# Kernel tuning notes

Hardware: AMD Instinct MI355X
Metric: run time of the kernel (lower is better)

Reference implementation:

```python
import jax, jax.numpy as jnp
import numpy as np

FRAMES = 8
NUM_HEADS = 12


def _build_indices_mask(N_origin):
    """Static (numpy) construction of gathered token indices and the
    multiplicative token mask (1.0 on allowed pairs, 0.8 elsewhere),
    matching token_mask + (1-token_mask)*0.8 in the torch code."""
    N = FRAMES * N_origin
    cls_idx = np.arange(0, N, N_origin)
    per_frame = [np.arange(i * N_origin + 1 + i, (i + 1) * N_origin, FRAMES)
                 for i in range(FRAMES)]
    idx = np.concatenate([cls_idx] + per_frame)
    M = idx.shape[0]
    mask = np.full((N, M), 0.8, dtype=np.float32)
    cls_len = cls_idx.shape[0]
    mask[:, :cls_len] = 1.0
    st = cls_len
    for i in range(FRAMES):
        ln = per_frame[i].shape[0]
        mask[i * N_origin:(i + 1) * N_origin, st:st + ln] = 1.0
        st += ln
    return jnp.asarray(idx), jnp.asarray(mask)


def setup_inputs() -> dict:
    key = jax.random.key(0)
    k1, k2, k3, k4 = jax.random.split(key, 4)
    C = 768
    x = jax.random.normal(k1, (64, 197, C), dtype=jnp.float32)
    qkv_w = jax.random.normal(k2, (3 * C, C), dtype=jnp.float32) * 0.02
    proj_w = jax.random.normal(k3, (C, C), dtype=jnp.float32) * 0.02
    proj_b = jax.random.normal(k4, (C,), dtype=jnp.float32) * 0.02
    return {"x": x, "qkv_w": qkv_w, "proj_w": proj_w, "proj_b": proj_b}


def reference(x, qkv_w, proj_w, proj_b):
    B0, N_origin, C = x.shape
    H = NUM_HEADS
    hd = C // H
    B = B0 // FRAMES
    N = FRAMES * N_origin
    scale = hd ** -0.5

    xg = x.reshape(B, N, C)                              # group 8 frames per video
    qkv = (xg @ qkv_w.T).reshape(B, N, 3, H, hd).transpose(2, 0, 3, 1, 4)
    q, k, v = qkv[0], qkv[1], qkv[2]                     # each [B, H, N, hd]

    idx, mask = _build_indices_mask(N_origin)            # idx [M], mask [N, M]
    k = k[:, :, idx, :]                                  # [B, H, M, hd]
    v = v[:, :, idx, :]

    attn = jnp.einsum('bhnd,bhmd->bhnm', q, k) * scale   # [B, H, N, M]
    attn = jax.nn.softmax(attn * mask, axis=-1)          # multiplicative mask, then softmax

    out = jnp.einsum('bhnm,bhmd->bhnd', attn, v)         # [B, H, N, hd]
    out = out.transpose(0, 2, 1, 3).reshape(B, N, C)
    out = out @ proj_w.T + proj_b
    return out.reshape(B0, N_origin, C)
```

## Files before the change

### kernel.cpp

```cpp
#include <hip/hip_runtime.h>
#include <stdint.h>

#define NORI   197
#define FRAMES 8
#define NTOK   1576
#define BATCH  8
#define NHEAD  12
#define CDIM   768
#define MG     204
#define TOKENS 12608

typedef _Float16 half8 __attribute__((ext_vector_type(8)));
typedef float floatx4 __attribute__((ext_vector_type(4)));

typedef const __attribute__((address_space(1))) void GPTR;
typedef __attribute__((address_space(3))) void LPTR;

__device__ __forceinline__ int gather_idx(int m) {
    if (m < 8) return m * NORI;
    int u = m - 8;
    int f, t;
    if (u < 100) { f = u / 25; t = u - f * 25; }
    else         { f = 4 + (u - 100) / 24; t = (u - 100) - (f - 4) * 24; }
    return f * NORI + 1 + f + 8 * t;
}
__device__ __forceinline__ int col_frame(int m) {
    int u = m - 8;
    return (u < 100) ? (u / 25) : (4 + (u - 100) / 24);
}

__global__ __launch_bounds__(256) void cast_all(
    const float* __restrict__ x, const float* __restrict__ qkvw,
    const float* __restrict__ projw, _Float16* __restrict__ out)
{
    const int n1 = TOKENS * CDIM / 8, n2 = 3 * CDIM * CDIM / 8, n3 = CDIM * CDIM / 8;
    int i = blockIdx.x * 256 + threadIdx.x;
    if (i >= n1 + n2 + n3) return;
    const float* src; int off;
    if (i < n1)           { src = x;     off = i; }
    else if (i < n1 + n2) { src = qkvw;  off = i - n1; }
    else                  { src = projw; off = i - n1 - n2; }
    float4 a = ((const float4*)src)[2 * off];
    float4 b = ((const float4*)src)[2 * off + 1];
    half8 o = { (_Float16)a.x, (_Float16)a.y, (_Float16)a.z, (_Float16)a.w,
                (_Float16)b.x, (_Float16)b.y, (_Float16)b.z, (_Float16)b.w };
    ((half8*)out)[i] = o;
}

template <int OUT_F32>
__device__ __forceinline__ void gemm_body64(
    const _Float16* __restrict__ A, const _Float16* __restrict__ W,
    const float* __restrict__ bias, void* __restrict__ Y,
    int M, int Woff, int ldY, int gather, int r0, int c0,
    _Float16* As0, _Float16* Bs0, _Float16* As1, _Float16* Bs1)
{
    const int tid = threadIdx.x;
    const int w = tid >> 6, l = tid & 63;
    const int wm = (w >> 1) * 32, wn = (w & 1) * 64;
    const int cg = (l & 3) ^ ((l >> 3) & 3);

    const _Float16* saA;
    {
        int rt = w * 16 + (l >> 2);
        int ra = min(r0 + rt, M - 1);
        if (gather) { int b = ra / MG; int m = ra - b * MG; ra = b * NTOK + gather_idx(m); }
        saA = A + (size_t)ra * CDIM + cg * 8;
    }
    const int soffA = (w * 16) * 32;

    const _Float16* sb[2];
    int soffB[2];
#pragma unroll
    for (int i = 0; i < 2; i++) {
        int rt = w * 32 + i * 16 + (l >> 2);
        sb[i] = W + (size_t)(Woff + c0 + rt) * CDIM + cg * 8;
        soffB[i] = (w * 32 + i * 16) * 32;
    }

    __builtin_amdgcn_global_load_lds((GPTR*)saA, (LPTR*)(As0 + soffA), 16, 0, 0);
#pragma unroll
    for (int i = 0; i < 2; i++)
        __builtin_amdgcn_global_load_lds((GPTR*)sb[i], (LPTR*)(Bs0 + soffB[i]), 16, 0, 0);

    floatx4 acc[2][4] = {};
    const int fc = ((l >> 4) ^ ((l >> 1) & 3)) * 8;
    const int mrow = l & 15;
    const int lm = l & 15, lq = l >> 4;

#pragma unroll
    for (int it = 0; it < 24; it++) {
        const _Float16* Ac = (it & 1) ? As1 : As0;
        const _Float16* Bc = (it & 1) ? Bs1 : Bs0;
        _Float16* An = (it & 1) ? As0 : As1;
        _Float16* Bn = (it & 1) ? Bs0 : Bs1;

        if (it < 23) {
            int kb = (it + 1) * 32;
            __builtin_amdgcn_global_load_lds((GPTR*)(saA + kb), (LPTR*)(An + soffA), 16, 0, 0);
#pragma unroll
            for (int i = 0; i < 2; i++)
                __builtin_amdgcn_global_load_lds((GPTR*)(sb[i] + kb), (LPTR*)(Bn + soffB[i]), 16, 0, 0);
            __builtin_amdgcn_s_waitcnt(0x0073);
        } else {
            __builtin_amdgcn_s_waitcnt(0x0070);
        }
        __builtin_amdgcn_s_barrier();
        __builtin_amdgcn_sched_barrier(0);

        half8 af[2], bf[4];
#pragma unroll
        for (int t = 0; t < 2; t++)
            af[t] = *(const half8*)&Ac[(wm + t * 16 + mrow) * 32 + fc];
#pragma unroll
        for (int t = 0; t < 4; t++)
            bf[t] = *(const half8*)&Bc[(wn + t * 16 + mrow) * 32 + fc];
#pragma unroll
        for (int mt = 0; mt < 2; mt++)
#pragma unroll
            for (int nt = 0; nt < 4; nt++)
                acc[mt][nt] = __builtin_amdgcn_mfma_f32_16x16x32_f16(af[mt], bf[nt], acc[mt][nt], 0, 0, 0);

        __builtin_amdgcn_sched_barrier(0);
        __builtin_amdgcn_s_barrier();
    }

#pragma unroll
    for (int nt = 0; nt < 4; nt++) {
        int col = c0 + wn + nt * 16 + lm;
        float bv = bias ? bias[col] : 0.f;
#pragma unroll
        for (int mt = 0; mt < 2; mt++) {
#pragma unroll
            for (int r = 0; r < 4; r++) {
                int row = r0 + wm + mt * 16 + lq * 4 + r;
                if (row < M) {
                    if (OUT_F32) ((float*)Y)[(size_t)row * ldY + col] = acc[mt][nt][r] + bv;
                    else ((_Float16*)Y)[(size_t)row * ldY + col] = (_Float16)acc[mt][nt][r];
                }
            }
        }
    }
}

__device__ __forceinline__ int xcd_chunk(int bid, int nwg) {
    int xcd = bid & 7, j = bid >> 3;
    int q = nwg >> 3, r = nwg & 7;
    int base = (xcd < r) ? xcd * (q + 1) : r * (q + 1) + (xcd - r) * q;
    return base + j;
}

__global__ __launch_bounds__(256, 5) void gemm_qkv(
    const _Float16* __restrict__ xh, const _Float16* __restrict__ qkvwh,
    _Float16* __restrict__ Qh, _Float16* __restrict__ KVh)
{
    __shared__ __align__(16) _Float16 As0[64 * 32];
    __shared__ __align__(16) _Float16 Bs0[128 * 32];
    __shared__ __align__(16) _Float16 As1[64 * 32];
    __shared__ __align__(16) _Float16 Bs1[128 * 32];
    int bx = blockIdx.x;
    if (bx < 1182) {
        int wg = xcd_chunk(bx, 1182);
        int rb = wg / 6, cb = wg - rb * 6;
        gemm_body64<0>(xh, qkvwh, nullptr, Qh, TOKENS, 0, CDIM, 0,
                       rb * 64, cb * 128, As0, Bs0, As1, Bs1);
    } else {
        int b2 = bx - 1182;
        int wg = xcd_chunk(b2, 312);
        int rb = wg / 12, cb = wg - rb * 12;
        gemm_body64<0>(xh, qkvwh, nullptr, KVh, BATCH * MG, CDIM, 1536, 1,
                       rb * 64, cb * 128, As0, Bs0, As1, Bs1);
    }
}

__global__ __launch_bounds__(256, 5) void gemm_proj(
    const _Float16* __restrict__ AOh, const _Float16* __restrict__ projwh,
    const float* __restrict__ bias, float* __restrict__ out)
{
    __shared__ __align__(16) _Float16 As0[64 * 32];
    __shared__ __align__(16) _Float16 Bs0[128 * 32];
    __shared__ __align__(16) _Float16 As1[64 * 32];
    __shared__ __align__(16) _Float16 Bs1[128 * 32];
    int wg = xcd_chunk(blockIdx.x, 1182);
    int rb = wg / 6, cb = wg - rb * 6;
    gemm_body64<1>(AOh, projwh, bias, out, TOKENS, 0, CDIM, 0,
                   rb * 64, cb * 128, As0, Bs0, As1, Bs1);
}

__global__ __launch_bounds__(256, 2) void attn_mfma(
    const _Float16* __restrict__ Qh, const _Float16* __restrict__ KVh,
    _Float16* __restrict__ AOh)
{
    __shared__ __align__(16) _Float16 Ks[204 * 64];
    __shared__ __align__(16) _Float16 Vt[64 * 208];
    __shared__ __align__(16) _Float16 Ps[64 * 216];

    const int tid = threadIdx.x;
    const int bh = blockIdx.x;
    const int b = bh / NHEAD, h = bh - b * NHEAD;
    const int qc0 = blockIdx.y * 320;

    for (int e = tid; e < MG * 8; e += 256) {
        int row = e >> 3, c8 = e & 7;
        half8 v = *(const half8*)&KVh[(size_t)(b * MG + row) * 1536 + h * 64 + c8 * 8];
        *(half8*)&Ks[row * 64 + ((c8 ^ (row & 7)) * 8)] = v;
    }
    {
        const int d0 = (tid >> 5) * 8, lmp = tid & 31;
#pragma unroll
        for (int mo = 0; mo < 7; mo++) {
            int mp = mo * 32 + lmp;
            if (mp >= 208) continue;
            half8 v = {};
            if (mp < MG) v = *(const half8*)&KVh[(size_t)(b * MG + mp) * 1536 + 768 + h * 64 + d0];
#pragma unroll
            for (int j = 0; j < 8; j++) Vt[(d0 + j) * 208 + mp] = v[j];
        }
    }
    __syncthreads();

    const int w = tid >> 6, l = tid & 63;
    const int lm = l & 15, lq = l >> 4;

    int cf[13];
#pragma unroll
    for (int t = 0; t < 13; t++) {
        int col = t * 16 + lm;
        cf[t] = (col < 8) ? -1 : (col >= MG ? -2 : col_frame(col));
    }

    _Float16* Pw = &Ps[(w * 16) * 216];

    for (int t5 = 0; t5 < 5; t5++) {
        const int rb = qc0 + t5 * 64 + w * 16;
        if (rb >= NTOK) break;

        floatx4 acc[13] = {};
        const int qrowA = min(rb + lm, NTOK - 1);
        const _Float16* qbase = Qh + (size_t)(b * NTOK + qrowA) * CDIM + h * 64;
        __builtin_amdgcn_s_setprio(1);
#pragma unroll
        for (int ks = 0; ks < 64; ks += 32) {
            half8 aq = *(const half8*)(qbase + ks + lq * 8);
#pragma unroll
            for (int t = 0; t < 13; t++) {
                half8 bk = *(const half8*)&Ks[(t * 16 + lm) * 64 + (((ks >> 3) + lq) ^ (lm & 7)) * 8];
                acc[t] = __builtin_amdgcn_mfma_f32_16x16x32_f16(aq, bk, acc[t], 0, 0, 0);
            }
        }
        __builtin_amdgcn_s_setprio(0);

#pragma unroll
        for (int r = 0; r < 4; r++) {
            int qrow = min(rb + lq * 4 + r, NTOK - 1);
            int rf = qrow / NORI;
            float sv[13];
            float mx = -1e30f;
#pragma unroll
            for (int t = 0; t < 13; t++) {
                float s = acc[t][r] * 0.125f;
                s *= (cf[t] == -1 || cf[t] == rf) ? 1.f : 0.8f;
                if (cf[t] == -2) s = -1e30f;
                sv[t] = s;
                mx = fmaxf(mx, s);
            }
#pragma unroll
            for (int off = 1; off < 16; off <<= 1) mx = fmaxf(mx, __shfl_xor(mx, off, 64));
            float sum = 0.f;
#pragma unroll
            for (int t = 0; t < 13; t++) { sv[t] = __expf(sv[t] - mx); sum += sv[t]; }
#pragma unroll
            for (int off = 1; off < 16; off <<= 1) sum += __shfl_xor(sum, off, 64);
            float inv = 1.f / sum;
#pragma unroll
            for (int t = 0; t < 13; t++) acc[t][r] = sv[t] * inv;
        }

#pragma unroll
        for (int t = 0; t < 13; t++)
#pragma unroll
            for (int r = 0; r < 4; r++)
                Pw[(lq * 4 + r) * 216 + t * 16 + lm] = (_Float16)acc[t][r];

        floatx4 oacc[4] = {};
        const _Float16* prow = &Pw[lm * 216];
        __builtin_amdgcn_s_setprio(1);
#pragma unroll
        for (int ks = 0; ks < 192; ks += 32) {
            half8 ap = *(const half8*)(prow + ks + lq * 8);
#pragma unroll
            for (int t = 0; t < 4; t++) {
                half8 bv = *(const half8*)&Vt[(t * 16 + lm) * 208 + ks + lq * 8];
                oacc[t] = __builtin_amdgcn_mfma_f32_16x16x32_f16(ap, bv, oacc[t], 0, 0, 0);
            }
        }
        {
            typedef _Float16 half4v __attribute__((ext_vector_type(4)));
            half4v ap4 = *(const half4v*)(prow + 192 + lq * 4);
#pragma unroll
            for (int t = 0; t < 4; t++) {
                half4v bv4 = *(const half4v*)&Vt[(t * 16 + lm) * 208 + 192 + lq * 4];
                oacc[t] = __builtin_amdgcn_mfma_f32_16x16x16f16(ap4, bv4, oacc[t], 0, 0, 0);
            }
        }
        __builtin_amdgcn_s_setprio(0);

#pragma unroll
        for (int t = 0; t < 4; t++)
#pragma unroll
            for (int r = 0; r < 4; r++) {
                int qrow = rb + lq * 4 + r;
                if (qrow < NTOK)
                    AOh[(size_t)(b * NTOK + qrow) * CDIM + h * 64 + t * 16 + lm] = (_Float16)oacc[t][r];
            }
    }
}

extern "C" void kernel_launch(void* const* d_in, const int* in_sizes, int n_in,
                              void* d_out, int out_size, void* d_ws, size_t ws_size,
                              hipStream_t stream) {
    const float* x      = (const float*)d_in[0];
    const float* qkv_w  = (const float*)d_in[1];
    const float* proj_w = (const float*)d_in[2];
    const float* proj_b = (const float*)d_in[3];
    float* out = (float*)d_out;

    _Float16* xh     = (_Float16*)d_ws;
    _Float16* qkvwh  = xh + (size_t)TOKENS * CDIM;
    _Float16* projwh = qkvwh + (size_t)3 * CDIM * CDIM;
    _Float16* Qh     = projwh + (size_t)CDIM * CDIM;
    _Float16* KVh    = Qh + (size_t)TOKENS * CDIM;
    _Float16* AOh    = KVh + (size_t)(BATCH * MG) * 1536;

    dim3 blk(256);
    const int ncast = (TOKENS * CDIM + 3 * CDIM * CDIM + CDIM * CDIM) / 8;
    cast_all<<<dim3((ncast + 255) / 256), blk, 0, stream>>>(x, qkv_w, proj_w, xh);

    gemm_qkv<<<dim3(1182 + 312), blk, 0, stream>>>(xh, qkvwh, Qh, KVh);

    attn_mfma<<<dim3(BATCH * NHEAD, 5), blk, 0, stream>>>(Qh, KVh, AOh);

    gemm_proj<<<dim3(1182), blk, 0, stream>>>(AOh, projwh, proj_b, out);
}
```

Before: 187.7 us.

## Triple-buffer GEMM shared-memory tiles with two-stage prefetch

Switches the QKV and projection GEMMs from double to triple buffering of the A/B LDS tiles, so each iteration issues loads two K-steps ahead and waits with an adjusted vmcnt. The aim is to hide more global-load latency behind MFMA work. It raises LDS use per block from 24KB to 36KB and lowers the launch-bounds occupancy hint from 5 to 4 blocks, which may cut latency hiding across waves.

```diff
diff --git a/kernel.cpp b/kernel.cpp
--- a/kernel.cpp
+++ b/kernel.cpp
@@ -47,12 +47,15 @@
     ((half8*)out)[i] = o;
 }
 
+#define ATS (64 * 32)
+#define BTS (128 * 32)
+
 template <int OUT_F32>
 __device__ __forceinline__ void gemm_body64(
     const _Float16* __restrict__ A, const _Float16* __restrict__ W,
     const float* __restrict__ bias, void* __restrict__ Y,
     int M, int Woff, int ldY, int gather, int r0, int c0,
-    _Float16* As0, _Float16* Bs0, _Float16* As1, _Float16* Bs1)
+    _Float16* As, _Float16* Bs)
 {
     const int tid = threadIdx.x;
     const int w = tid >> 6, l = tid & 63;
@@ -77,10 +80,14 @@
         soffB[i] = (w * 32 + i * 16) * 32;
     }
 
-    __builtin_amdgcn_global_load_lds((GPTR*)saA, (LPTR*)(As0 + soffA), 16, 0, 0);
-#pragma unroll
-    for (int i = 0; i < 2; i++)
-        __builtin_amdgcn_global_load_lds((GPTR*)sb[i], (LPTR*)(Bs0 + soffB[i]), 16, 0, 0);
+#pragma unroll
+    for (int p = 0; p < 2; p++) {
+        int kb = p * 32;
+        __builtin_amdgcn_global_load_lds((GPTR*)(saA + kb), (LPTR*)(As + p * ATS + soffA), 16, 0, 0);
+#pragma unroll
+        for (int i = 0; i < 2; i++)
+            __builtin_amdgcn_global_load_lds((GPTR*)(sb[i] + kb), (LPTR*)(Bs + p * BTS + soffB[i]), 16, 0, 0);
+    }
 
     floatx4 acc[2][4] = {};
     const int fc = ((l >> 4) ^ ((l >> 1) & 3)) * 8;
@@ -89,17 +96,18 @@
 
 #pragma unroll
     for (int it = 0; it < 24; it++) {
-        const _Float16* Ac = (it & 1) ? As1 : As0;
-        const _Float16* Bc = (it & 1) ? Bs1 : Bs0;
-        _Float16* An = (it & 1) ? As0 : As1;
-        _Float16* Bn = (it & 1) ? Bs0 : Bs1;
-
-        if (it < 23) {
-            int kb = (it + 1) * 32;
-            __builtin_amdgcn_global_load_lds((GPTR*)(saA + kb), (LPTR*)(An + soffA), 16, 0, 0);
+        const _Float16* Ac = As + (it % 3) * ATS;
+        const _Float16* Bc = Bs + (it % 3) * BTS;
+
+        if (it < 22) {
+            int kb = (it + 2) * 32;
+            int p = (it + 2) % 3;
+            __builtin_amdgcn_global_load_lds((GPTR*)(saA + kb), (LPTR*)(As + p * ATS + soffA), 16, 0, 0);
 #pragma unroll
             for (int i = 0; i < 2; i++)
-                __builtin_amdgcn_global_load_lds((GPTR*)(sb[i] + kb), (LPTR*)(Bn + soffB[i]), 16, 0, 0);
+                __builtin_amdgcn_global_load_lds((GPTR*)(sb[i] + kb), (LPTR*)(Bs + p * BTS + soffB[i]), 16, 0, 0);
+            __builtin_amdgcn_s_waitcnt(0x0076);
+        } else if (it == 22) {
             __builtin_amdgcn_s_waitcnt(0x0073);
         } else {
             __builtin_amdgcn_s_waitcnt(0x0070);
@@ -149,41 +157,37 @@
     return base + j;
 }
 
-__global__ __launch_bounds__(256, 5) void gemm_qkv(
+__global__ __launch_bounds__(256, 4) void gemm_qkv(
     const _Float16* __restrict__ xh, const _Float16* __restrict__ qkvwh,
     _Float16* __restrict__ Qh, _Float16* __restrict__ KVh)
 {
-    __shared__ __align__(16) _Float16 As0[64 * 32];
-    __shared__ __align__(16) _Float16 Bs0[128 * 32];
-    __shared__ __align__(16) _Float16 As1[64 * 32];
-    __shared__ __align__(16) _Float16 Bs1[128 * 32];
+    __shared__ __align__(16) _Float16 As[3 * ATS];
+    __shared__ __align__(16) _Float16 Bs[3 * BTS];
     int bx = blockIdx.x;
     if (bx < 1182) {
         int wg = xcd_chunk(bx, 1182);
         int rb = wg / 6, cb = wg - rb * 6;
         gemm_body64<0>(xh, qkvwh, nullptr, Qh, TOKENS, 0, CDIM, 0,
-                       rb * 64, cb * 128, As0, Bs0, As1, Bs1);
+                       rb * 64, cb * 128, As, Bs);
     } else {
         int b2 = bx - 1182;
         int wg = xcd_chunk(b2, 312);
         int rb = wg / 12, cb = wg - rb * 12;
         gemm_body64<0>(xh, qkvwh, nullptr, KVh, BATCH * MG, CDIM, 1536, 1,
-                       rb * 64, cb * 128, As0, Bs0, As1, Bs1);
-    }
-}
-
-__global__ __launch_bounds__(256, 5) void gemm_proj(
+                       rb * 64, cb * 128, As, Bs);
+    }
+}
+
+__global__ __launch_bounds__(256, 4) void gemm_proj(
     const _Float16* __restrict__ AOh, const _Float16* __restrict__ projwh,
     const float* __restrict__ bias, float* __restrict__ out)
 {
-    __shared__ __align__(16) _Float16 As0[64 * 32];
-    __shared__ __align__(16) _Float16 Bs0[128 * 32];
-    __shared__ __align__(16) _Float16 As1[64 * 32];
-    __shared__ __align__(16) _Float16 Bs1[128 * 32];
+    __shared__ __align__(16) _Float16 As[3 * ATS];
+    __shared__ __align__(16) _Float16 Bs[3 * BTS];
     int wg = xcd_chunk(blockIdx.x, 1182);
     int rb = wg / 6, cb = wg - rb * 6;
     gemm_body64<1>(AOh, projwh, bias, out, TOKENS, 0, CDIM, 0,
-                   rb * 64, cb * 128, As0, Bs0, As1, Bs1);
+                   rb * 64, cb * 128, As, Bs);
 }
 
 __global__ __launch_bounds__(256, 2) void attn_mfma(
```

New measurement: 197.2 us. 5.1% more time.

## Replace LDS-staged GEMM with direct global-to-register MFMA loads and 128x128 tiles

Applied to the files above, without the earlier changes.

Rewrites the QKV and projection GEMM bodies to load MFMA fragments directly from global memory into registers, dropping the LDS double buffer and barriers. The tile grows to 128x128 per block, with 4x4 MFMA accumulators per wave, halving the grid size. This removes LDS traffic and synchronisation but gives up cross-wave sharing of loaded tiles and explicit prefetch, relying on caches to absorb the redundant global loads.

```diff
diff --git a/kernel.cpp b/kernel.cpp
--- a/kernel.cpp
+++ b/kernel.cpp
@@ -12,9 +12,6 @@
 
 typedef _Float16 half8 __attribute__((ext_vector_type(8)));
 typedef float floatx4 __attribute__((ext_vector_type(4)));
-
-typedef const __attribute__((address_space(1))) void GPTR;
-typedef __attribute__((address_space(3))) void LPTR;
 
 __device__ __forceinline__ int gather_idx(int m) {
     if (m < 8) return m * NORI;
@@ -48,80 +45,44 @@
 }
 
 template <int OUT_F32>
-__device__ __forceinline__ void gemm_body64(
+__device__ __forceinline__ void gemm_body_reg(
     const _Float16* __restrict__ A, const _Float16* __restrict__ W,
     const float* __restrict__ bias, void* __restrict__ Y,
-    int M, int Woff, int ldY, int gather, int r0, int c0,
-    _Float16* As0, _Float16* Bs0, _Float16* As1, _Float16* Bs1)
+    int M, int Woff, int ldY, int gather, int r0, int c0)
 {
     const int tid = threadIdx.x;
     const int w = tid >> 6, l = tid & 63;
-    const int wm = (w >> 1) * 32, wn = (w & 1) * 64;
-    const int cg = (l & 3) ^ ((l >> 3) & 3);
-
-    const _Float16* saA;
-    {
-        int rt = w * 16 + (l >> 2);
-        int ra = min(r0 + rt, M - 1);
-        if (gather) { int b = ra / MG; int m = ra - b * MG; ra = b * NTOK + gather_idx(m); }
-        saA = A + (size_t)ra * CDIM + cg * 8;
-    }
-    const int soffA = (w * 16) * 32;
-
-    const _Float16* sb[2];
-    int soffB[2];
-#pragma unroll
-    for (int i = 0; i < 2; i++) {
-        int rt = w * 32 + i * 16 + (l >> 2);
-        sb[i] = W + (size_t)(Woff + c0 + rt) * CDIM + cg * 8;
-        soffB[i] = (w * 32 + i * 16) * 32;
-    }
-
-    __builtin_amdgcn_global_load_lds((GPTR*)saA, (LPTR*)(As0 + soffA), 16, 0, 0);
-#pragma unroll
-    for (int i = 0; i < 2; i++)
-        __builtin_amdgcn_global_load_lds((GPTR*)sb[i], (LPTR*)(Bs0 + soffB[i]), 16, 0, 0);
-
-    floatx4 acc[2][4] = {};
-    const int fc = ((l >> 4) ^ ((l >> 1) & 3)) * 8;
-    const int mrow = l & 15;
+    const int wm = (w >> 1) * 64, wn = (w & 1) * 64;
     const int lm = l & 15, lq = l >> 4;
 
+    const _Float16* pa[4];
+#pragma unroll
+    for (int t = 0; t < 4; t++) {
+        int row = min(r0 + wm + t * 16 + lm, M - 1);
+        if (gather) { int b = row / MG; int m = row - b * MG; row = b * NTOK + gather_idx(m); }
+        pa[t] = A + (size_t)row * CDIM + lq * 8;
+    }
+    const _Float16* pb[4];
+#pragma unroll
+    for (int t = 0; t < 4; t++) {
+        int col = c0 + wn + t * 16 + lm;
+        pb[t] = W + (size_t)(Woff + col) * CDIM + lq * 8;
+    }
+
+    floatx4 acc[4][4] = {};
+
 #pragma unroll
     for (int it = 0; it < 24; it++) {
-        const _Float16* Ac = (it & 1) ? As1 : As0;
-        const _Float16* Bc = (it & 1) ? Bs1 : Bs0;
-        _Float16* An = (it & 1) ? As0 : As1;
-        _Float16* Bn = (it & 1) ? Bs0 : Bs1;
-
-        if (it < 23) {
-            int kb = (it + 1) * 32;
-            __builtin_amdgcn_global_load_lds((GPTR*)(saA + kb), (LPTR*)(An + soffA), 16, 0, 0);
-#pragma unroll
-            for (int i = 0; i < 2; i++)
-                __builtin_amdgcn_global_load_lds((GPTR*)(sb[i] + kb), (LPTR*)(Bn + soffB[i]), 16, 0, 0);
-            __builtin_amdgcn_s_waitcnt(0x0073);
-        } else {
-            __builtin_amdgcn_s_waitcnt(0x0070);
-        }
-        __builtin_amdgcn_s_barrier();
-        __builtin_amdgcn_sched_barrier(0);
-
-        half8 af[2], bf[4];
-#pragma unroll
-        for (int t = 0; t < 2; t++)
-            af[t] = *(const half8*)&Ac[(wm + t * 16 + mrow) * 32 + fc];
-#pragma unroll
-        for (int t = 0; t < 4; t++)
-            bf[t] = *(const half8*)&Bc[(wn + t * 16 + mrow) * 32 + fc];
-#pragma unroll
-        for (int mt = 0; mt < 2; mt++)
+        half8 af[4], bf[4];
+#pragma unroll
+        for (int t = 0; t < 4; t++) af[t] = *(const half8*)(pa[t] + it * 32);
+#pragma unroll
+        for (int t = 0; t < 4; t++) bf[t] = *(const half8*)(pb[t] + it * 32);
+#pragma unroll
+        for (int mt = 0; mt < 4; mt++)
 #pragma unroll
             for (int nt = 0; nt < 4; nt++)
                 acc[mt][nt] = __builtin_amdgcn_mfma_f32_16x16x32_f16(af[mt], bf[nt], acc[mt][nt], 0, 0, 0);
-
-        __builtin_amdgcn_sched_barrier(0);
-        __builtin_amdgcn_s_barrier();
     }
 
 #pragma unroll
@@ -129,7 +90,7 @@
         int col = c0 + wn + nt * 16 + lm;
         float bv = bias ? bias[col] : 0.f;
 #pragma unroll
-        for (int mt = 0; mt < 2; mt++) {
+        for (int mt = 0; mt < 4; mt++) {
 #pragma unroll
             for (int r = 0; r < 4; r++) {
                 int row = r0 + wm + mt * 16 + lq * 4 + r;
@@ -149,41 +110,33 @@
     return base + j;
 }
 
-__global__ __launch_bounds__(256, 5) void gemm_qkv(
+__global__ __launch_bounds__(256, 2) void gemm_qkv(
     const _Float16* __restrict__ xh, const _Float16* __restrict__ qkvwh,
     _Float16* __restrict__ Qh, _Float16* __restrict__ KVh)
 {
-    __shared__ __align__(16) _Float16 As0[64 * 32];
-    __shared__ __align__(16) _Float16 Bs0[128 * 32];
-    __shared__ __align__(16) _Float16 As1[64 * 32];
-    __shared__ __align__(16) _Float16 Bs1[128 * 32];
     int bx = blockIdx.x;
-    if (bx < 1182) {
-        int wg = xcd_chunk(bx, 1182);
+    if (bx < 594) {
+        int wg = xcd_chunk(bx, 594);
         int rb = wg / 6, cb = wg - rb * 6;
-        gemm_body64<0>(xh, qkvwh, nullptr, Qh, TOKENS, 0, CDIM, 0,
-                       rb * 64, cb * 128, As0, Bs0, As1, Bs1);
+        gemm_body_reg<0>(xh, qkvwh, nullptr, Qh, TOKENS, 0, CDIM, 0,
+                         rb * 128, cb * 128);
     } else {
-        int b2 = bx - 1182;
-        int wg = xcd_chunk(b2, 312);
+        int b2 = bx - 594;
+        int wg = xcd_chunk(b2, 156);
         int rb = wg / 12, cb = wg - rb * 12;
-        gemm_body64<0>(xh, qkvwh, nullptr, KVh, BATCH * MG, CDIM, 1536, 1,
-                       rb * 64, cb * 128, As0, Bs0, As1, Bs1);
-    }
-}
-
-__global__ __launch_bounds__(256, 5) void gemm_proj(
+        gemm_body_reg<0>(xh, qkvwh, nullptr, KVh, BATCH * MG, CDIM, 1536, 1,
+                         rb * 128, cb * 128);
+    }
+}
+
+__global__ __launch_bounds__(256, 2) void gemm_proj(
     const _Float16* __restrict__ AOh, const _Float16* __restrict__ projwh,
     const float* __restrict__ bias, float* __restrict__ out)
 {
-    __shared__ __align__(16) _Float16 As0[64 * 32];
-    __shared__ __align__(16) _Float16 Bs0[128 * 32];
-    __shared__ __align__(16) _Float16 As1[64 * 32];
-    __shared__ __align__(16) _Float16 Bs1[128 * 32];
-    int wg = xcd_chunk(blockIdx.x, 1182);
+    int wg = xcd_chunk(blockIdx.x, 594);
     int rb = wg / 6, cb = wg - rb * 6;
-    gemm_body64<1>(AOh, projwh, bias, out, TOKENS, 0, CDIM, 0,
-                   rb * 64, cb * 128, As0, Bs0, As1, Bs1);
+    gemm_body_reg<1>(AOh, projwh, bias, out, TOKENS, 0, CDIM, 0,
+                     rb * 128, cb * 128);
 }
 
 __global__ __launch_bounds__(256, 2) void attn_mfma(
@@ -335,9 +288,9 @@
     const int ncast = (TOKENS * CDIM + 3 * CDIM * CDIM + CDIM * CDIM) / 8;
     cast_all<<<dim3((ncast + 255) / 256), blk, 0, stream>>>(x, qkv_w, proj_w, xh);
 
-    gemm_qkv<<<dim3(1182 + 312), blk, 0, stream>>>(xh, qkvwh, Qh, KVh);
+    gemm_qkv<<<dim3(594 + 156), blk, 0, stream>>>(xh, qkvwh, Qh, KVh);
 
     attn_mfma<<<dim3(BATCH * NHEAD, 5), blk, 0, stream>>>(Qh, KVh, AOh);
 
-    gemm_proj<<<dim3(1182), blk, 0, stream>>>(AOh, projwh, proj_b, out);
-}
+    gemm_proj<<<dim3(594), blk, 0, stream>>>(AOh, projwh, proj_b, out);
+}
```

Result: slower. 265.7 us (+41.6%).
